# Performance work log

Hardware: AMD Instinct MI355X
Metric: run time of the kernel (lower is better)

The kernel has to match this reference:

```python
import jax, jax.numpy as jnp
import numpy as np

EPS = 1e-5   # torch BatchNorm2d default eps
HEADS = 4


def conv1x1_bn(x, w, g, b, m, v):
    # 1x1 conv (no bias) == channel matmul, then inference-mode BatchNorm
    y = jnp.einsum('oc,bchw->bohw', w, x)
    s = g / jnp.sqrt(v + EPS)
    return y * s[None, :, None, None] + (b - m * s)[None, :, None, None]


def dwconv3x3_bn(x, w, g, b, m, v):
    # depthwise 3x3 conv, padding 1 (autopad), groups=C, then BatchNorm
    C = x.shape[1]
    y = jax.lax.conv_general_dilated(
        x, w, window_strides=(1, 1), padding=((1, 1), (1, 1)),
        dimension_numbers=('NCHW', 'OIHW', 'NCHW'), feature_group_count=C)
    s = g / jnp.sqrt(v + EPS)
    return y * s[None, :, None, None] + (b - m * s)[None, :, None, None]


def split_heads(x):
    b, c, h, w = x.shape
    hd = c // HEADS
    return x.reshape(b, HEADS, hd, h * w).transpose(0, 1, 3, 2)  # [b,heads,n,hd]


def merge_heads(x, h, w):
    b, heads, n, hd = x.shape
    return x.transpose(0, 1, 3, 2).reshape(b, heads * hd, h, w)


def setup_inputs() -> dict:
    key = jax.random.key(0)
    B, C, H, W = 4, 256, 48, 48
    ks = jax.random.split(key, 32)
    inp = {
        'q': jax.random.normal(ks[0], (B, C, H, W), jnp.float32),
        'k': jax.random.normal(ks[1], (B, C, H, W), jnp.float32),
        'v': jax.random.normal(ks[2], (B, C, H, W), jnp.float32),
    }
    i = 3
    for name in ['wq', 'wk', 'wv', 'proj']:
        inp[name + '_w'] = jax.random.normal(ks[i], (C, C), jnp.float32) * 0.02; i += 1
    inp['pe_w'] = jax.random.normal(ks[i], (C, 1, 3, 3), jnp.float32) * 0.1; i += 1
    for name in ['wq', 'wk', 'wv', 'pe', 'proj']:
        inp[name + '_g'] = jax.random.uniform(ks[i], (C,), jnp.float32, 0.5, 1.5); i += 1
        inp[name + '_b'] = jax.random.normal(ks[i], (C,), jnp.float32) * 0.1; i += 1
        inp[name + '_m'] = jax.random.normal(ks[i], (C,), jnp.float32) * 0.1; i += 1
        inp[name + '_v'] = jax.random.uniform(ks[i], (C,), jnp.float32, 0.5, 1.5); i += 1
    return inp


def reference(q, k, v,
              wq_w, wk_w, wv_w, proj_w, pe_w,
              wq_g, wq_b, wq_m, wq_v,
              wk_g, wk_b, wk_m, wk_v,
              wv_g, wv_b, wv_m, wv_v,
              pe_g, pe_b, pe_m, pe_v,
              proj_g, proj_b, proj_m, proj_v):
    H, W = q.shape[2], q.shape[3]
    qf = conv1x1_bn(q, wq_w, wq_g, wq_b, wq_m, wq_v)
    kf = conv1x1_bn(k, wk_w, wk_g, wk_b, wk_m, wk_v)
    vf = conv1x1_bn(v, wv_w, wv_g, wv_b, wv_m, wv_v)
    qh = split_heads(qf)  # [b,heads,n,hd]
    kh = split_heads(kf)
    vh = split_heads(vf)
    scale = qh.shape[-1] ** -0.5
    attn = jax.nn.softmax(jnp.einsum('bhnd,bhmd->bhnm', qh, kh) * scale, axis=-1)
    y = jnp.einsum('bhnm,bhmd->bhnd', attn, vh)
    y = merge_heads(y, H, W) + dwconv3x3_bn(merge_heads(qh, H, W), pe_w, pe_g, pe_b, pe_m, pe_v)
    return conv1x1_bn(y, proj_w, proj_g, proj_b, proj_m, proj_v)
```

## Files before the change

### kernel.cpp

```cpp
#include <hip/hip_runtime.h>
#include <math.h>

#define HEADS 4
#define HD    64
#define CCH   256
#define NB    4
#define HH    48
#define WW    48
#define NN    (HH*WW)
#define EPSBN 1e-5f
#define KSCL  0.18033688f
#define BCN   (NB*CCH*NN)
#define NSP   4

typedef unsigned short ushort_t;
typedef __attribute__((ext_vector_type(8))) short bfrag;
typedef __attribute__((ext_vector_type(4))) float f32x4;
typedef __attribute__((ext_vector_type(16))) float f32x16;

#define MFMA   __builtin_amdgcn_mfma_f32_16x16x32_bf16
#define MFMA32 __builtin_amdgcn_mfma_f32_32x32x16_bf16

static __device__ __forceinline__ unsigned cvtpk(float lo, float hi) {
    unsigned r;
    asm("v_cvt_pk_bf16_f32 %0, %1, %2" : "=v"(r) : "v"(lo), "v"(hi));
    return r;
}
static __device__ __forceinline__ float fexp2(float x) {
    float r;
    asm("v_exp_f32 %0, %1" : "=v"(r) : "v"(x));
    return r;
}
static __device__ __forceinline__ float bflo(unsigned u) { return __uint_as_float(u << 16); }
static __device__ __forceinline__ float bfhi(unsigned u) { return __uint_as_float(u & 0xffff0000u); }

static __device__ __forceinline__ void gload16(const void* g, void* l) {
    __builtin_amdgcn_global_load_lds(
        (const __attribute__((address_space(1))) void*)g,
        (__attribute__((address_space(3))) void*)l, 16, 0, 0);
}

static __device__ __forceinline__ ushort_t f2bf(float x) {
    unsigned int u = __float_as_uint(x);
    unsigned int r = (u + 0x7fffu + ((u >> 16) & 1u)) >> 16;
    return (ushort_t)r;
}

struct ConvP {
    const float* X0; const float* X1; const float* X2;
    const ushort_t* T;
    const float* W[4]; const float* G[4]; const float* Bb[4];
    const float* Mm[4]; const float* Vv[4];
    const float* pew; const float* peg; const float* peb;
    const float* pem; const float* pev;
    ushort_t* pw2; float* pbias;
    ushort_t* qnd; ushort_t* knd; ushort_t* vcn; float* outf;
};

template<int PROJ>
__global__ __launch_bounds__(512)
void conv_gemm(ConvP P)
{
    __shared__ ushort_t Ts[64][264];
    __shared__ ushort_t Ws[64][264];
    const int nt = blockIdx.x, ot = blockIdx.y, z = blockIdx.z;
    const int tid = threadIdx.x;
    if (!PROJ && z == 12) {
        if (nt == 0 && ot == 0 && tid < CCH) {
            int c = tid;
            float s = P.peg[c] * rsqrtf(P.pev[c] + EPSBN);
            for (int tap = 0; tap < 9; ++tap)
                P.pw2[tap * CCH + c] = f2bf(P.pew[c * 9 + tap] * s);
            P.pbias[c] = P.peb[c] - P.pem[c] * s;
        }
        return;
    }
    const int which = PROJ ? 3 : (z >> 2);
    const int b = z & 3;
    const int n0 = nt * 64, o0 = ot * 64;
    const float* Wf  = P.W[which];
    const float* Gf  = P.G[which];
    const float* Bbf = P.Bb[which];
    const float* Mmf = P.Mm[which];
    const float* Vvf = P.Vv[which];
    const float wmul = (which == 1) ? KSCL : 1.0f;

#pragma unroll
    for (int i = 0; i < 4; ++i) {
        int idx = tid + i * 512;
        int r = idx >> 5, c16 = idx & 31;
        int o = o0 + r;
        float s2 = Gf[o] * rsqrtf(Vvf[o] + EPSBN) * wmul;
        const float* wp = Wf + (size_t)o * CCH + c16 * 8;
        float4 wa = *(const float4*)&wp[0];
        float4 wb = *(const float4*)&wp[4];
        uint4 u;
        u.x = cvtpk(wa.x * s2, wa.y * s2); u.y = cvtpk(wa.z * s2, wa.w * s2);
        u.z = cvtpk(wb.x * s2, wb.y * s2); u.w = cvtpk(wb.z * s2, wb.w * s2);
        *(uint4*)&Ws[r][c16 * 8] = u;
    }
    if (!PROJ) {
        const float* Xf = (which == 0) ? P.X0 : (which == 1) ? P.X1 : P.X2;
        const float* Xb = Xf + (size_t)b * CCH * NN + n0;
        const int n = tid & 63;
#pragma unroll
        for (int p = 0; p < 4; ++p) {
            int c0 = (tid >> 6) * 8 + p * 64;
            const float* src = Xb + (size_t)c0 * NN + n;
            float vv[8];
#pragma unroll
            for (int j = 0; j < 8; ++j) vv[j] = src[(size_t)j * NN];
            uint4 u;
            u.x = cvtpk(vv[0], vv[1]); u.y = cvtpk(vv[2], vv[3]);
            u.z = cvtpk(vv[4], vv[5]); u.w = cvtpk(vv[6], vv[7]);
            *(uint4*)&Ts[n][c0] = u;
        }
    } else {
        const ushort_t* Tsrc = P.T + ((size_t)b * NN + n0) * CCH;
#pragma unroll
        for (int i = 0; i < 4; ++i) {
            int idx = tid + i * 512;
            int r = idx >> 5, c16 = idx & 31;
            *(uint4*)&Ts[r][c16 * 8] = *(const uint4*)&Tsrc[(size_t)r * CCH + c16 * 8];
        }
    }
    __syncthreads();
    const int wv = tid >> 6, lane = tid & 63, lr = lane & 15, lg = lane >> 4;
    const int qn = (wv >> 1) * 16, qo = (wv & 1) * 32;
    f32x4 acc[2];
    acc[0] = (f32x4){0.f, 0.f, 0.f, 0.f};
    acc[1] = (f32x4){0.f, 0.f, 0.f, 0.f};

    if (!PROJ && which < 2) {
#pragma unroll
        for (int k8 = 0; k8 < 8; ++k8) {
            const int kc = k8 * 32 + lg * 8;
            bfrag ta  = *(const bfrag*)&Ts[qn + lr][kc];
            bfrag wa0 = *(const bfrag*)&Ws[qo + lr][kc];
            bfrag wa1 = *(const bfrag*)&Ws[qo + 16 + lr][kc];
            acc[0] = MFMA(ta, wa0, acc[0], 0, 0, 0);
            acc[1] = MFMA(ta, wa1, acc[1], 0, 0, 0);
        }
    } else {
#pragma unroll
        for (int k8 = 0; k8 < 8; ++k8) {
            const int kc = k8 * 32 + lg * 8;
            bfrag ta  = *(const bfrag*)&Ts[qn + lr][kc];
            bfrag wa0 = *(const bfrag*)&Ws[qo + lr][kc];
            bfrag wa1 = *(const bfrag*)&Ws[qo + 16 + lr][kc];
            acc[0] = MFMA(wa0, ta, acc[0], 0, 0, 0);
            acc[1] = MFMA(wa1, ta, acc[1], 0, 0, 0);
        }
    }

    __syncthreads();
    if (!PROJ && which < 2) {
        ushort_t (*Ot)[72] = (ushort_t(*)[72])Ts;
        float bv[2];
#pragma unroll
        for (int j = 0; j < 2; ++j) {
            int o = o0 + qo + j * 16 + lr;
            float s = Gf[o] * rsqrtf(Vvf[o] + EPSBN);
            bv[j] = (Bbf[o] - Mmf[o] * s) * wmul;
        }
#pragma unroll
        for (int j = 0; j < 2; ++j)
#pragma unroll
            for (int r = 0; r < 4; ++r)
                Ot[qn + lg * 4 + r][qo + j * 16 + lr] = f2bf(acc[j][r] + bv[j]);
        __syncthreads();
        ushort_t* out = (which == 0) ? P.qnd : P.knd;
        {
            int r = tid >> 3, sg = tid & 7;
            *(uint4*)&out[(((size_t)b * HEADS + ot) * NN + n0 + r) * HD + sg * 8] =
                *(const uint4*)&Ot[r][sg * 8];
        }
    } else if (!PROJ) {
        ushort_t (*Ot)[72] = (ushort_t(*)[72])Ts;
#pragma unroll
        for (int j = 0; j < 2; ++j)
#pragma unroll
            for (int r = 0; r < 4; ++r) {
                int o = o0 + qo + j * 16 + lg * 4 + r;
                float s = Gf[o] * rsqrtf(Vvf[o] + EPSBN);
                float bv = Bbf[o] - Mmf[o] * s;
                Ot[qo + j * 16 + lg * 4 + r][qn + lr] = f2bf(acc[j][r] + bv);
            }
        __syncthreads();
        {
            int r = tid >> 3, sg = tid & 7;
            *(uint4*)&P.vcn[((size_t)b * CCH + o0 + r) * NN + n0 + sg * 8] =
                *(const uint4*)&Ot[r][sg * 8];
        }
    } else {
        float (*Of)[68] = (float(*)[68])Ts;
#pragma unroll
        for (int j = 0; j < 2; ++j)
#pragma unroll
            for (int r = 0; r < 4; ++r) {
                int o = o0 + qo + j * 16 + lg * 4 + r;
                float s = Gf[o] * rsqrtf(Vvf[o] + EPSBN);
                float bv = Bbf[o] - Mmf[o] * s;
                Of[qo + j * 16 + lg * 4 + r][qn + lr] = acc[j][r] + bv;
            }
        __syncthreads();
#pragma unroll
        for (int i = 0; i < 2; ++i) {
            int idx = tid + i * 512;
            int r = idx >> 4, c4 = idx & 15;
            *(float4*)&P.outf[((size_t)b * CCH + o0 + r) * NN + n0 + c4 * 4] =
                *(const float4*)&Of[r][c4 * 4];
        }
    }
}

__global__ __launch_bounds__(256, 4)
void attn_kernel(const ushort_t* __restrict__ Qnd,
                 const ushort_t* __restrict__ Knd,
                 const ushort_t* __restrict__ Vcn,
                 ushort_t* __restrict__ Op,
                 float* __restrict__ Larr)
{
    __shared__ __align__(16) char smem[32768];

    const int tid = threadIdx.x;
    const int lin0 = blockIdx.x + 18 * blockIdx.y + 288 * blockIdx.z;
    const int w    = (lin0 & 7) * 144 + (lin0 >> 3);
    const int qt = w % 18;
    const int bh = (w / 18) & 15;
    const int sp = w / 288;
    const int b = bh >> 2, h = bh & 3;
    const int lane = tid & 63, wv = tid >> 6;
    const int l31 = lane & 31, hi = lane >> 5, l7 = lane & 7;
    const int lrow = lane >> 3, lslot = (lane & 7) ^ lrow;
    const int n0 = qt * 128;
    const size_t ndb = (size_t)(b * HEADS + h) * NN * HD;
    const size_t cnb = ((size_t)b * CCH + h * HD) * NN;

    const char* kgp = (const char*)(Knd + ndb) + (size_t)(sp * 576 + wv * 16 + lrow) * 128 + lslot * 16;
    const char* vgp = (const char*)(Vcn + cnb + sp * 576) + (size_t)(wv * 16 + lrow) * (NN * 2) + lslot * 16;
    char* kls = smem + wv * 2048;
    char* vls = smem + 16384 + wv * 2048;

#define STAGE(buf, t) do { \
    const char* kp_ = kgp + (size_t)(t) * 8192; \
    const char* vp_ = vgp + (size_t)(t) * 128; \
    char* kd_ = kls + (buf) * 8192; \
    char* vd_ = vls + (buf) * 8192; \
    gload16(kp_,              kd_); \
    gload16(kp_ + 1024,       kd_ + 1024); \
    gload16(vp_,              vd_); \
    gload16(vp_ + 8 * (NN*2), vd_ + 1024); \
} while (0)

    bfrag qb[4];
    {
        const ushort_t* qbase = Qnd + ndb + (size_t)(n0 + wv * 32 + l31) * HD + hi * 8;
#pragma unroll
        for (int ds = 0; ds < 4; ++ds)
            qb[ds] = *(const bfrag*)&qbase[ds * 16];
    }

    f32x16 o[2];
#pragma unroll
    for (int db = 0; db < 2; ++db)
#pragma unroll
        for (int j = 0; j < 16; ++j) o[db][j] = 0.f;
    float lacc0 = 0.f, lacc1 = 0.f;

    STAGE(0, 0);

    for (int t = 0; t < 9; ++t) {
        const int cur = t & 1;
        asm volatile("s_waitcnt vmcnt(0)" ::: "memory");
        __builtin_amdgcn_s_barrier();
        if (t < 8) STAGE(cur ^ 1, t + 1);
        const char* Kb = smem + cur * 8192;
        const char* Vb = smem + 16384 + cur * 8192;

        bfrag pf[4];
#pragma unroll
        for (int kb = 0; kb < 2; ++kb) {
            f32x16 s;
#pragma unroll
            for (int j = 0; j < 16; ++j) s[j] = 0.f;
            __builtin_amdgcn_s_setprio(1);
#pragma unroll
            for (int ds = 0; ds < 4; ++ds) {
                const char* ka_p = Kb + (kb * 32 + l31) * 128 + (((2 * ds + hi) ^ l7) << 4);
                bfrag ka = *(const bfrag*)ka_p;
                s = MFMA32(ka, qb[ds], s, 0, 0, 0);
            }
            __builtin_amdgcn_s_setprio(0);
            float e[16];
#pragma unroll
            for (int j = 0; j < 16; ++j) e[j] = fexp2(s[j]);
#pragma unroll
            for (int j = 0; j < 8; ++j) { lacc0 += e[2 * j]; lacc1 += e[2 * j + 1]; }
            unsigned u[4][2];
#pragma unroll
            for (int g = 0; g < 4; ++g) {
                u[g][0] = cvtpk(e[4 * g + 0], e[4 * g + 1]);
                u[g][1] = cvtpk(e[4 * g + 2], e[4 * g + 3]);
            }
#pragma unroll
            for (int ks = 0; ks < 2; ++ks) {
                asm("v_permlane32_swap_b32 %0, %1" : "+v"(u[2*ks][0]), "+v"(u[2*ks+1][0]));
                asm("v_permlane32_swap_b32 %0, %1" : "+v"(u[2*ks][1]), "+v"(u[2*ks+1][1]));
                uint4 fw = { u[2*ks][0], u[2*ks][1], u[2*ks+1][0], u[2*ks+1][1] };
                pf[kb * 2 + ks] = *(const bfrag*)&fw;
            }
        }

        __builtin_amdgcn_s_setprio(1);
#pragma unroll
        for (int db = 0; db < 2; ++db)
#pragma unroll
            for (int ks = 0; ks < 4; ++ks) {
                const char* va_p = Vb + (db * 32 + l31) * 128 + (((2 * ks + hi) ^ l7) << 4);
                bfrag va = *(const bfrag*)va_p;
                o[db] = MFMA32(va, pf[ks], o[db], 0, 0, 0);
            }
        __builtin_amdgcn_s_setprio(0);
    }
#undef STAGE
    __builtin_amdgcn_s_barrier();

    float lacc = lacc0 + lacc1;
    lacc += __shfl_xor(lacc, 32);
    if (hi == 0)
        Larr[(size_t)(sp * 16 + bh) * NN + n0 + wv * 32 + l31] = lacc;

    unsigned (*Osb)[36] = (unsigned(*)[36])smem;
    {
        int row = wv * 32 + l31;
#pragma unroll
        for (int db = 0; db < 2; ++db)
#pragma unroll
            for (int g = 0; g < 4; ++g) {
                uint2 pk;
                pk.x = cvtpk(o[db][4 * g + 0], o[db][4 * g + 1]);
                pk.y = cvtpk(o[db][4 * g + 2], o[db][4 * g + 3]);
                *(uint2*)&Osb[row][16 * db + 4 * g + 2 * hi] = pk;
            }
    }
    __syncthreads();
    ushort_t* opb = Op + (size_t)sp * BCN + ((size_t)b * NN + n0) * CCH + h * HD;
    for (int idx = tid; idx < 1024; idx += 256) {
        int n = idx >> 3, s4 = idx & 7;
        *(uint4*)&opb[(size_t)n * CCH + s4 * 8] = *(const uint4*)&Osb[n][s4 * 4];
    }
}

__global__ __launch_bounds__(256)
void fuse_kernel(const ushort_t* __restrict__ Op, const float* __restrict__ Larr,
                 const ushort_t* __restrict__ Qnd,
                 const ushort_t* __restrict__ pw2, const float* __restrict__ pbias,
                 ushort_t* __restrict__ yt)
{
    const int tid = threadIdx.x;
    const int b  = blockIdx.x / 288;
    const int n0 = (blockIdx.x % 288) * 8;
    const int c8 = tid & 31, ns = tid >> 5;
    const int n  = n0 + ns;
    const int h  = c8 >> 3, c0 = c8 * 8;

    const ushort_t* o0p = Op + ((size_t)b * NN + n) * CCH + c0;
    float acc[8] = {0.f, 0.f, 0.f, 0.f, 0.f, 0.f, 0.f, 0.f};
#pragma unroll
    for (int s = 0; s < NSP; ++s) {
        uint4 u = *(const uint4*)&o0p[(size_t)s * BCN];
        acc[0] += bflo(u.x); acc[1] += bfhi(u.x);
        acc[2] += bflo(u.y); acc[3] += bfhi(u.y);
        acc[4] += bflo(u.z); acc[5] += bfhi(u.z);
        acc[6] += bflo(u.w); acc[7] += bfhi(u.w);
    }
    int mi = (b * HEADS + h) * NN + n;
    float ls = 0.f;
#pragma unroll
    for (int s = 0; s < NSP; ++s) ls += Larr[(size_t)s * 16 * NN + mi];
    float rinv = 1.0f / ls;
#pragma unroll
    for (int j = 0; j < 8; ++j) acc[j] *= rinv;

    const int x = n % WW, y = n / WW;
    const ushort_t* qb = Qnd + (size_t)(b * HEADS + h) * NN * HD + (c8 & 7) * 8;
#pragma unroll
    for (int ky = 0; ky < 3; ++ky) {
        int yy = y + ky - 1;
        if (yy < 0 || yy >= HH) continue;
#pragma unroll
        for (int kx = 0; kx < 3; ++kx) {
            int xx = x + kx - 1;
            if (xx < 0 || xx >= WW) continue;
            int np = yy * WW + xx;
            uint4 qv = *(const uint4*)&qb[(size_t)np * HD];
            uint4 w4 = *(const uint4*)&pw2[(ky * 3 + kx) * CCH + c0];
            acc[0] += bflo(qv.x) * bflo(w4.x); acc[1] += bfhi(qv.x) * bfhi(w4.x);
            acc[2] += bflo(qv.y) * bflo(w4.y); acc[3] += bfhi(qv.y) * bfhi(w4.y);
            acc[4] += bflo(qv.z) * bflo(w4.z); acc[5] += bfhi(qv.z) * bfhi(w4.z);
            acc[6] += bflo(qv.w) * bflo(w4.w); acc[7] += bfhi(qv.w) * bfhi(w4.w);
        }
    }
    float4 p0 = *(const float4*)&pbias[c0];
    float4 p1 = *(const float4*)&pbias[c0 + 4];
    acc[0] += p0.x; acc[1] += p0.y; acc[2] += p0.z; acc[3] += p0.w;
    acc[4] += p1.x; acc[5] += p1.y; acc[6] += p1.z; acc[7] += p1.w;
    uint4 u;
    u.x = cvtpk(acc[0], acc[1]); u.y = cvtpk(acc[2], acc[3]);
    u.z = cvtpk(acc[4], acc[5]); u.w = cvtpk(acc[6], acc[7]);
    *(uint4*)&yt[((size_t)b * NN + n) * CCH + c0] = u;
}

extern "C" void kernel_launch(void* const* d_in, const int* in_sizes, int n_in,
                              void* d_out, int out_size, void* d_ws, size_t ws_size,
                              hipStream_t stream) {
    char* ws = (char*)d_ws;
    ushort_t* qnd  = (ushort_t*)(ws + 0);
    ushort_t* knd  = (ushort_t*)(ws + 4718592);
    ushort_t* vcn  = (ushort_t*)(ws + 9437184);
    ushort_t* Op   = (ushort_t*)(ws + 14155776);
    ushort_t* yt   = (ushort_t*)(ws + 4718592);
    float*    Larr = (float*)   (ws + 33030144);
    ushort_t* pw2  = (ushort_t*)(ws + 33619968);
    float*    pbias= (float*)   (ws + 33624576);

    ConvP P;
    P.X0 = (const float*)d_in[0];
    P.X1 = (const float*)d_in[1];
    P.X2 = (const float*)d_in[2];
    P.T  = yt;
    P.W[0] = (const float*)d_in[3]; P.W[1] = (const float*)d_in[4];
    P.W[2] = (const float*)d_in[5]; P.W[3] = (const float*)d_in[6];
    P.G[0]  = (const float*)d_in[8];  P.Bb[0] = (const float*)d_in[9];
    P.Mm[0] = (const float*)d_in[10]; P.Vv[0] = (const float*)d_in[11];
    P.G[1]  = (const float*)d_in[12]; P.Bb[1] = (const float*)d_in[13];
    P.Mm[1] = (const float*)d_in[14]; P.Vv[1] = (const float*)d_in[15];
    P.G[2]  = (const float*)d_in[16]; P.Bb[2] = (const float*)d_in[17];
    P.Mm[2] = (const float*)d_in[18]; P.Vv[2] = (const float*)d_in[19];
    P.G[3]  = (const float*)d_in[24]; P.Bb[3] = (const float*)d_in[25];
    P.Mm[3] = (const float*)d_in[26]; P.Vv[3] = (const float*)d_in[27];
    P.pew = (const float*)d_in[7];
    P.peg = (const float*)d_in[20]; P.peb = (const float*)d_in[21];
    P.pem = (const float*)d_in[22]; P.pev = (const float*)d_in[23];
    P.pw2 = pw2; P.pbias = pbias;
    P.qnd = qnd; P.knd = knd; P.vcn = vcn; P.outf = (float*)d_out;

    conv_gemm<0><<<dim3(36, 4, 13), 512, 0, stream>>>(P);

    attn_kernel<<<dim3(18, 16, NSP), 256, 0, stream>>>(qnd, knd, vcn, Op, Larr);

    fuse_kernel<<<1152, 256, 0, stream>>>(Op, Larr, qnd, pw2, pbias, yt);

    conv_gemm<1><<<dim3(36, 4, 4), 512, 0, stream>>>(P);
}
```

Baseline: 76.76 us.

## Process two query sub-tiles per wave in attention to reuse K/V fragments

Each attention wave now handles 64 query rows (two 32-row chunks) instead of 32, so every K and V fragment loaded from LDS feeds two MFMAs. The block covers 256 queries, which halves the grid and the total global K/V staging traffic. The cost is roughly doubled accumulator and fragment registers, a lower occupancy hint (2 blocks instead of 4), a larger shared buffer, and only 576 blocks left to spread across the GPU.

```diff
diff --git a/kernel.cpp b/kernel.cpp
--- a/kernel.cpp
+++ b/kernel.cpp
@@ -214,26 +214,26 @@
     }
 }
 
-__global__ __launch_bounds__(256, 4)
+__global__ __launch_bounds__(256, 2)
 void attn_kernel(const ushort_t* __restrict__ Qnd,
                  const ushort_t* __restrict__ Knd,
                  const ushort_t* __restrict__ Vcn,
                  ushort_t* __restrict__ Op,
                  float* __restrict__ Larr)
 {
-    __shared__ __align__(16) char smem[32768];
+    __shared__ __align__(16) char smem[40960];
 
     const int tid = threadIdx.x;
-    const int lin0 = blockIdx.x + 18 * blockIdx.y + 288 * blockIdx.z;
-    const int w    = (lin0 & 7) * 144 + (lin0 >> 3);
-    const int qt = w % 18;
-    const int bh = (w / 18) & 15;
-    const int sp = w / 288;
+    const int lin0 = blockIdx.x + 9 * blockIdx.y + 144 * blockIdx.z;
+    const int w    = (lin0 & 7) * 72 + (lin0 >> 3);
+    const int qt = w % 9;
+    const int bh = (w / 9) & 15;
+    const int sp = w / 144;
     const int b = bh >> 2, h = bh & 3;
     const int lane = tid & 63, wv = tid >> 6;
     const int l31 = lane & 31, hi = lane >> 5, l7 = lane & 7;
     const int lrow = lane >> 3, lslot = (lane & 7) ^ lrow;
-    const int n0 = qt * 128;
+    const int n0 = qt * 256;
     const size_t ndb = (size_t)(b * HEADS + h) * NN * HD;
     const size_t cnb = ((size_t)b * CCH + h * HD) * NN;
 
@@ -253,20 +253,26 @@
     gload16(vp_ + 8 * (NN*2), vd_ + 1024); \
 } while (0)
 
-    bfrag qb[4];
+    bfrag qb[2][4];
     {
-        const ushort_t* qbase = Qnd + ndb + (size_t)(n0 + wv * 32 + l31) * HD + hi * 8;
-#pragma unroll
-        for (int ds = 0; ds < 4; ++ds)
-            qb[ds] = *(const bfrag*)&qbase[ds * 16];
-    }
-
-    f32x16 o[2];
-#pragma unroll
-    for (int db = 0; db < 2; ++db)
-#pragma unroll
-        for (int j = 0; j < 16; ++j) o[db][j] = 0.f;
-    float lacc0 = 0.f, lacc1 = 0.f;
+#pragma unroll
+        for (int qc = 0; qc < 2; ++qc) {
+            const ushort_t* qbase = Qnd + ndb
+                + (size_t)(n0 + wv * 64 + qc * 32 + l31) * HD + hi * 8;
+#pragma unroll
+            for (int ds = 0; ds < 4; ++ds)
+                qb[qc][ds] = *(const bfrag*)&qbase[ds * 16];
+        }
+    }
+
+    f32x16 o[2][2];
+#pragma unroll
+    for (int qc = 0; qc < 2; ++qc)
+#pragma unroll
+        for (int db = 0; db < 2; ++db)
+#pragma unroll
+            for (int j = 0; j < 16; ++j) o[qc][db][j] = 0.f;
+    float lacc0[2] = {0.f, 0.f}, lacc1[2] = {0.f, 0.f};
 
     STAGE(0, 0);
 
@@ -278,37 +284,41 @@
         const char* Kb = smem + cur * 8192;
         const char* Vb = smem + 16384 + cur * 8192;
 
-        bfrag pf[4];
+        bfrag pf[2][4];
 #pragma unroll
         for (int kb = 0; kb < 2; ++kb) {
-            f32x16 s;
-#pragma unroll
-            for (int j = 0; j < 16; ++j) s[j] = 0.f;
+            f32x16 s0, s1;
+#pragma unroll
+            for (int j = 0; j < 16; ++j) { s0[j] = 0.f; s1[j] = 0.f; }
             __builtin_amdgcn_s_setprio(1);
 #pragma unroll
             for (int ds = 0; ds < 4; ++ds) {
                 const char* ka_p = Kb + (kb * 32 + l31) * 128 + (((2 * ds + hi) ^ l7) << 4);
                 bfrag ka = *(const bfrag*)ka_p;
-                s = MFMA32(ka, qb[ds], s, 0, 0, 0);
+                s0 = MFMA32(ka, qb[0][ds], s0, 0, 0, 0);
+                s1 = MFMA32(ka, qb[1][ds], s1, 0, 0, 0);
             }
             __builtin_amdgcn_s_setprio(0);
-            float e[16];
-#pragma unroll
-            for (int j = 0; j < 16; ++j) e[j] = fexp2(s[j]);
-#pragma unroll
-            for (int j = 0; j < 8; ++j) { lacc0 += e[2 * j]; lacc1 += e[2 * j + 1]; }
-            unsigned u[4][2];
-#pragma unroll
-            for (int g = 0; g < 4; ++g) {
-                u[g][0] = cvtpk(e[4 * g + 0], e[4 * g + 1]);
-                u[g][1] = cvtpk(e[4 * g + 2], e[4 * g + 3]);
-            }
-#pragma unroll
-            for (int ks = 0; ks < 2; ++ks) {
-                asm("v_permlane32_swap_b32 %0, %1" : "+v"(u[2*ks][0]), "+v"(u[2*ks+1][0]));
-                asm("v_permlane32_swap_b32 %0, %1" : "+v"(u[2*ks][1]), "+v"(u[2*ks+1][1]));
-                uint4 fw = { u[2*ks][0], u[2*ks][1], u[2*ks+1][0], u[2*ks+1][1] };
-                pf[kb * 2 + ks] = *(const bfrag*)&fw;
+#pragma unroll
+            for (int qc = 0; qc < 2; ++qc) {
+                float e[16];
+#pragma unroll
+                for (int j = 0; j < 16; ++j) e[j] = fexp2(qc ? s1[j] : s0[j]);
+#pragma unroll
+                for (int j = 0; j < 8; ++j) { lacc0[qc] += e[2 * j]; lacc1[qc] += e[2 * j + 1]; }
+                unsigned u[4][2];
+#pragma unroll
+                for (int g = 0; g < 4; ++g) {
+                    u[g][0] = cvtpk(e[4 * g + 0], e[4 * g + 1]);
+                    u[g][1] = cvtpk(e[4 * g + 2], e[4 * g + 3]);
+                }
+#pragma unroll
+                for (int ks = 0; ks < 2; ++ks) {
+                    asm("v_permlane32_swap_b32 %0, %1" : "+v"(u[2*ks][0]), "+v"(u[2*ks+1][0]));
+                    asm("v_permlane32_swap_b32 %0, %1" : "+v"(u[2*ks][1]), "+v"(u[2*ks+1][1]));
+                    uint4 fw = { u[2*ks][0], u[2*ks][1], u[2*ks+1][0], u[2*ks+1][1] };
+                    pf[qc][kb * 2 + ks] = *(const bfrag*)&fw;
+                }
             }
         }
 
@@ -319,34 +329,39 @@
             for (int ks = 0; ks < 4; ++ks) {
                 const char* va_p = Vb + (db * 32 + l31) * 128 + (((2 * ks + hi) ^ l7) << 4);
                 bfrag va = *(const bfrag*)va_p;
-                o[db] = MFMA32(va, pf[ks], o[db], 0, 0, 0);
+                o[0][db] = MFMA32(va, pf[0][ks], o[0][db], 0, 0, 0);
+                o[1][db] = MFMA32(va, pf[1][ks], o[1][db], 0, 0, 0);
             }
         __builtin_amdgcn_s_setprio(0);
     }
 #undef STAGE
     __builtin_amdgcn_s_barrier();
 
-    float lacc = lacc0 + lacc1;
-    lacc += __shfl_xor(lacc, 32);
-    if (hi == 0)
-        Larr[(size_t)(sp * 16 + bh) * NN + n0 + wv * 32 + l31] = lacc;
-
-    unsigned (*Osb)[36] = (unsigned(*)[36])smem;
-    {
-        int row = wv * 32 + l31;
+#pragma unroll
+    for (int qc = 0; qc < 2; ++qc) {
+        float lacc = lacc0[qc] + lacc1[qc];
+        lacc += __shfl_xor(lacc, 32);
+        if (hi == 0)
+            Larr[(size_t)(sp * 16 + bh) * NN + n0 + wv * 64 + qc * 32 + l31] = lacc;
+    }
+
+    unsigned (*Osb)[40] = (unsigned(*)[40])smem;
+#pragma unroll
+    for (int qc = 0; qc < 2; ++qc) {
+        int row = wv * 64 + qc * 32 + l31;
 #pragma unroll
         for (int db = 0; db < 2; ++db)
 #pragma unroll
             for (int g = 0; g < 4; ++g) {
                 uint2 pk;
-                pk.x = cvtpk(o[db][4 * g + 0], o[db][4 * g + 1]);
-                pk.y = cvtpk(o[db][4 * g + 2], o[db][4 * g + 3]);
+                pk.x = cvtpk(o[qc][db][4 * g + 0], o[qc][db][4 * g + 1]);
+                pk.y = cvtpk(o[qc][db][4 * g + 2], o[qc][db][4 * g + 3]);
                 *(uint2*)&Osb[row][16 * db + 4 * g + 2 * hi] = pk;
             }
     }
     __syncthreads();
     ushort_t* opb = Op + (size_t)sp * BCN + ((size_t)b * NN + n0) * CCH + h * HD;
-    for (int idx = tid; idx < 1024; idx += 256) {
+    for (int idx = tid; idx < 2048; idx += 256) {
         int n = idx >> 3, s4 = idx & 7;
         *(uint4*)&opb[(size_t)n * CCH + s4 * 8] = *(const uint4*)&Osb[n][s4 * 4];
     }
@@ -448,7 +463,7 @@
 
     conv_gemm<0><<<dim3(36, 4, 13), 512, 0, stream>>>(P);
 
-    attn_kernel<<<dim3(18, 16, NSP), 256, 0, stream>>>(qnd, knd, vcn, Op, Larr);
+    attn_kernel<<<dim3(9, 16, NSP), 256, 0, stream>>>(qnd, knd, vcn, Op, Larr);
 
     fuse_kernel<<<1152, 256, 0, stream>>>(Op, Larr, qnd, pw2, pbias, yt);
 
```

Measured after the change: 78.18 us. No clear change (+1.8%).
